# Performance work log

Measured on AMD Instinct MI355X. Metric: run time of the kernel, lower is better.

The kernel has to match this reference:

```python
import jax, jax.numpy as jnp
import numpy as np

N = 1024   # nodes (genomic bins); batch must be 1 per the original reshape
F = 128    # input feature dim
Fp = 64    # F_ per head
H = 2      # attn heads
NEG = -1e16


def setup_inputs() -> dict:
    key = jax.random.key(0)
    ks = jax.random.split(key, 6)
    X = jax.random.normal(ks[0], (1, N, F), dtype=jnp.float32)
    A = (jax.random.uniform(ks[1], (1, N, N)) < 0.05).astype(jnp.float32)
    W1 = jax.random.normal(ks[2], (H, F, Fp), dtype=jnp.float32) * (1.0 / np.sqrt(F))
    W2 = jax.random.normal(ks[3], (H, F, Fp), dtype=jnp.float32) * (1.0 / np.sqrt(F))
    b = jax.random.normal(ks[4], (H, Fp), dtype=jnp.float32) * 0.02
    a_att = jax.random.normal(ks[5], (H, Fp), dtype=jnp.float32) * (1.0 / np.sqrt(Fp))
    return {"X": X, "A": A, "W1": W1, "W2": W2, "b": b, "a_att": a_att}


def reference(X, A, W1, W2, b, a_att):
    # Per-head projections (vectorized over heads): [1, H, N, Fp]
    HW1 = jnp.einsum('bnf,hfe->bhne', X, W1)
    HW2 = jnp.einsum('bnf,hfe->bhne', X, W2)
    # Pairwise broadcast: pair[b,h,i,j,:] = HW1[i] + HW2[j] + bias  -> [1,H,N,N,Fp]
    pair = HW1[:, :, :, None, :] + HW2[:, :, None, :, :] + b[None, :, None, None, :]
    f = jax.nn.leaky_relu(pair, negative_slope=0.2)
    # Attention logits: project with attn kernel -> [1,H,N,N]
    att = jnp.einsum('bhije,he->bhij', f, a_att)
    # Mask non-edges, sigmoid attention (NOT softmax), custom normalization
    att = att + NEG * (1.0 - A)[:, None, :, :]
    att = jax.nn.sigmoid(att)
    att_sum = jnp.sum(att, axis=-1, keepdims=True)        # [1,H,N,1]
    att = att / (1.0 + att_sum)
    beta = 1.0 / (1.0 + att_sum)                          # self (promoter) weight
    # Aggregate: beta * HW1 + att @ HW2 (dropout is identity at inference)
    out = beta * HW1 + jnp.einsum('bhij,bhje->bhie', att, HW2)
    # Concat heads along feature dim: [1, N, H*Fp]
    out = jnp.transpose(out, (0, 2, 1, 3)).reshape(X.shape[0], X.shape[1], -1)
    out = jax.nn.relu(out)
    return out, att
```

## Files before the change

### kernel.cpp

```cpp
#include <hip/hip_runtime.h>

#define NN 1024
#define FF 128
#define FP 64
#define NH 2

#define VT_OFF 0
#define H2_OFF 131072
#define SV_OFF 262144
#define FLAG_OFF (1 << 22)
#define GEN 0x9E3779B1u

__device__ __forceinline__ void st_ag2(float* p, float x, float y) {
    union { unsigned long long u; float f[2]; } c;
    c.f[0] = x; c.f[1] = y;
    __hip_atomic_store((unsigned long long*)p, c.u, __ATOMIC_RELAXED,
                       __HIP_MEMORY_SCOPE_AGENT);
}
__device__ __forceinline__ void st_ag1(float* p, float x) {
    union { unsigned u; float f; } c; c.f = x;
    __hip_atomic_store((unsigned*)p, c.u, __ATOMIC_RELAXED,
                       __HIP_MEMORY_SCOPE_AGENT);
}

__global__ __launch_bounds__(512) void kFused(const float* __restrict__ X,
        const float* __restrict__ Ad, const float* __restrict__ W1,
        const float* __restrict__ W2, const float* __restrict__ b,
        const float* __restrict__ a, float* __restrict__ ws,
        float* __restrict__ out, float* __restrict__ att) {
    union Shm {
        float xs[8 * FF];
        struct { float eval[8][256]; int eidx[8][256]; } p2;
    };
    __shared__ Shm shm;
    __shared__ float s_u[FP][8];
    __shared__ float s_h1[8][FP];
    __shared__ float s_ae[FP];
    __shared__ float s_su[8];
    __shared__ __align__(16) float s_att[8][NN];
    __shared__ float s_rsum[8][8];
    __shared__ float s_inv[8];

    int h    = blockIdx.x >> 7;
    int i0   = (blockIdx.x & 127) * 8;
    int t    = threadIdx.x;
    int lane = t & 63;
    int wv   = t >> 6;

    *(float2*)(shm.xs + t * 2) = *(const float2*)(X + i0 * FF + t * 2);
    if (t < FP) s_ae[t] = a[h * FP + t];
    __syncthreads();

    {
        int wsel = wv >> 2;
        int r0   = (wv & 3) * 2;
        const float* Wp = (wsel ? W2 : W1) + h * FF * FP;
        const float* x0 = shm.xs + (r0 + 0) * FF;
        const float* x1 = shm.xs + (r0 + 1) * FF;
        float acc0 = 0.f, acc1 = 0.f;
        #pragma unroll 8
        for (int f = 0; f < FF; f += 4) {
            float w0 = Wp[(f + 0) * FP + lane];
            float w1 = Wp[(f + 1) * FP + lane];
            float w2 = Wp[(f + 2) * FP + lane];
            float w3 = Wp[(f + 3) * FP + lane];
            float4 xa = *(const float4*)(x0 + f);
            float4 xb = *(const float4*)(x1 + f);
            acc0 += w0 * xa.x + w1 * xa.y + w2 * xa.z + w3 * xa.w;
            acc1 += w0 * xb.x + w1 * xb.y + w2 * xb.z + w3 * xb.w;
        }
        float be = wsel ? 0.f : b[h * FP + lane];
        float u0 = acc0 + be, u1 = acc1 + be;
        float ae = s_ae[lane];
        float g0 = ae * u0, g1 = ae * u1;
        #pragma unroll
        for (int off = 32; off; off >>= 1) {
            g0 += __shfl_xor(g0, off, 64);
            g1 += __shfl_xor(g1, off, 64);
        }
        if (wsel == 0) {
            s_u[lane][r0] = u0; s_u[lane][r0 + 1] = u1;
            s_h1[r0][lane] = acc0; s_h1[r0 + 1][lane] = acc1;
            if (lane == 0) { s_su[r0] = g0; s_su[r0 + 1] = g1; }
        } else {
            st_ag2(ws + VT_OFF + h * FP * NN + lane * NN + i0 + r0, u0, u1);
            float* H2g = ws + H2_OFF + (h * NN + i0 + r0) * FP;
            st_ag1(H2g + lane, acc0);
            st_ag1(H2g + FP + lane, acc1);
            if (lane == 0)
                st_ag2(ws + SV_OFF + h * NN + i0 + r0, g0, g1);
        }
    }

    __syncthreads();
    unsigned int* flags = (unsigned int*)(ws + FLAG_OFF);
    if (t == 0)
        __hip_atomic_store(&flags[blockIdx.x], GEN, __ATOMIC_RELAXED,
                           __HIP_MEMORY_SCOPE_AGENT);
    if (t < 256) {
        while (__hip_atomic_load(&flags[t], __ATOMIC_RELAXED,
                                 __HIP_MEMORY_SCOPE_AGENT) != GEN)
            __builtin_amdgcn_s_sleep(4);
    }
    asm volatile("" ::: "memory");
    __syncthreads();

    int j2 = t * 2;
    float2 A2r[8];
    #pragma unroll
    for (int ii = 0; ii < 8; ++ii)
        A2r[ii] = *(const float2*)(Ad + (i0 + ii) * NN + j2);
    float2 sv = *(const float2*)(ws + SV_OFF + h * NN + j2);

    const float* VTp = ws + VT_OFF + h * FP * NN + j2;
    float acc[16];
    #pragma unroll
    for (int k = 0; k < 16; ++k) acc[k] = 0.f;

    #pragma unroll 8
    for (int e = 0; e < FP; ++e) {
        float2 v = *(const float2*)(VTp + e * NN);
        float4 ua = *(const float4*)(&s_u[e][0]);
        float4 ub = *(const float4*)(&s_u[e][4]);
        float ae = s_ae[e];
        float uu[8] = {ua.x, ua.y, ua.z, ua.w, ub.x, ub.y, ub.z, ub.w};
        #pragma unroll
        for (int ii = 0; ii < 8; ++ii) {
            acc[ii * 2 + 0] += ae * fabsf(uu[ii] + v.x);
            acc[ii * 2 + 1] += ae * fabsf(uu[ii] + v.y);
        }
    }

    float rs[8];
    #pragma unroll
    for (int ii = 0; ii < 8; ++ii) {
        float l0 = 0.6f * (s_su[ii] + sv.x) + 0.4f * acc[ii * 2 + 0];
        float l1 = 0.6f * (s_su[ii] + sv.y) + 0.4f * acc[ii * 2 + 1];
        float s0 = (A2r[ii].x != 0.f) ? 1.f / (1.f + __expf(-l0)) : 0.f;
        float s1 = (A2r[ii].y != 0.f) ? 1.f / (1.f + __expf(-l1)) : 0.f;
        acc[ii * 2 + 0] = s0;
        acc[ii * 2 + 1] = s1;
        *(float2*)(&s_att[ii][j2]) = make_float2(s0, s1);
        rs[ii] = s0 + s1;
    }
    #pragma unroll
    for (int off = 32; off; off >>= 1) {
        #pragma unroll
        for (int ii = 0; ii < 8; ++ii) rs[ii] += __shfl_xor(rs[ii], off, 64);
    }
    if (lane == 0) {
        #pragma unroll
        for (int ii = 0; ii < 8; ++ii) s_rsum[wv][ii] = rs[ii];
    }
    __syncthreads();
    if (t < 8) {
        float S = 0.f;
        #pragma unroll
        for (int wq = 0; wq < 8; ++wq) S += s_rsum[wq][t];
        s_inv[t] = 1.f / (1.f + S);
    }
    __syncthreads();

    #pragma unroll
    for (int ii = 0; ii < 8; ++ii) {
        float iv = s_inv[ii];
        *(float2*)(att + (h * NN + i0 + ii) * NN + j2) =
            make_float2(acc[ii * 2 + 0] * iv, acc[ii * 2 + 1] * iv);
    }

    int cnt = 0;
    #pragma unroll
    for (int c = 0; c < 16; ++c) {
        float val = s_att[wv][c * 64 + lane];
        unsigned long long m = __ballot(val != 0.f);
        if (val != 0.f) {
            int pos = cnt + __popcll(m & ((1ull << lane) - 1ull));
            if (pos < 256) {
                shm.p2.eidx[wv][pos] = c * 64 + lane;
                shm.p2.eval[wv][pos] = val;
            }
        }
        cnt += __popcll(m);
    }
    if (cnt > 256) cnt = 256;

    const float* H2p = ws + H2_OFF + h * NN * FP + lane;
    float agg = 0.f;
    #pragma unroll 4
    for (int k = 0; k < cnt; ++k) {
        agg += shm.p2.eval[wv][k] * H2p[shm.p2.eidx[wv][k] * FP];
    }
    float h1  = s_h1[wv][lane];
    float val = s_inv[wv] * (h1 + agg);
    out[(i0 + wv) * (NH * FP) + h * FP + lane] = fmaxf(val, 0.f);
}

extern "C" void kernel_launch(void* const* d_in, const int* in_sizes, int n_in,
                              void* d_out, int out_size, void* d_ws, size_t ws_size,
                              hipStream_t stream) {
    const float* X  = (const float*)d_in[0];
    const float* A  = (const float*)d_in[1];
    const float* W1 = (const float*)d_in[2];
    const float* W2 = (const float*)d_in[3];
    const float* b  = (const float*)d_in[4];
    const float* a  = (const float*)d_in[5];

    float* out = (float*)d_out;
    float* att = out + NN * NH * FP;
    float* ws  = (float*)d_ws;

    kFused<<<256, 512, 0, stream>>>(X, A, W1, W2, b, a, ws, out, att);
}
```

Baseline: 35.59 us.

## Stage VT tiles through double-buffered shared memory with register prefetch

Replaces direct per-thread global float2 loads of the transposed projection VT with cooperative float4 loads into a double-buffered LDS tile of 4 feature rows. The next tile is prefetched into registers while the current one is consumed, then written to the other buffer. The aim is wider coalesced global loads and hiding load latency. In exchange it adds 16 block-wide barriers and extra LDS traffic, and the data is only read once per thread anyway.

```diff
diff --git a/kernel.cpp b/kernel.cpp
--- a/kernel.cpp
+++ b/kernel.cpp
@@ -30,6 +30,7 @@
         float* __restrict__ out, float* __restrict__ att) {
     union Shm {
         float xs[8 * FF];
+        float vt[2 * 4 * NN];
         struct { float eval[8][256]; int eidx[8][256]; } p2;
     };
     __shared__ Shm shm;
@@ -112,23 +113,46 @@
         A2r[ii] = *(const float2*)(Ad + (i0 + ii) * NN + j2);
     float2 sv = *(const float2*)(ws + SV_OFF + h * NN + j2);
 
-    const float* VTp = ws + VT_OFF + h * FP * NN + j2;
+    const float* VTg = ws + VT_OFF + h * FP * NN;
     float acc[16];
     #pragma unroll
     for (int k = 0; k < 16; ++k) acc[k] = 0.f;
 
-    #pragma unroll 8
-    for (int e = 0; e < FP; ++e) {
-        float2 v = *(const float2*)(VTp + e * NN);
-        float4 ua = *(const float4*)(&s_u[e][0]);
-        float4 ub = *(const float4*)(&s_u[e][4]);
-        float ae = s_ae[e];
-        float uu[8] = {ua.x, ua.y, ua.z, ua.w, ub.x, ub.y, ub.z, ub.w};
-        #pragma unroll
-        for (int ii = 0; ii < 8; ++ii) {
-            acc[ii * 2 + 0] += ae * fabsf(uu[ii] + v.x);
-            acc[ii * 2 + 1] += ae * fabsf(uu[ii] + v.y);
-        }
+    {
+        const float4* s = (const float4*)VTg;
+        float4 pa = s[t], pb = s[t + 512];
+        ((float4*)shm.vt)[t] = pa;
+        ((float4*)shm.vt)[t + 512] = pb;
+    }
+    __syncthreads();
+
+    for (int c = 0; c < 16; ++c) {
+        int cur = c & 1;
+        float4 na, nb;
+        if (c < 15) {
+            const float4* s = (const float4*)(VTg + (c + 1) * 4096);
+            na = s[t]; nb = s[t + 512];
+        }
+        #pragma unroll
+        for (int eq = 0; eq < 4; ++eq) {
+            int e = c * 4 + eq;
+            float2 v = *(const float2*)(&shm.vt[cur * 4096 + eq * NN + j2]);
+            float4 ua = *(const float4*)(&s_u[e][0]);
+            float4 ub = *(const float4*)(&s_u[e][4]);
+            float ae = s_ae[e];
+            float uu[8] = {ua.x, ua.y, ua.z, ua.w, ub.x, ub.y, ub.z, ub.w};
+            #pragma unroll
+            for (int ii = 0; ii < 8; ++ii) {
+                acc[ii * 2 + 0] += ae * fabsf(uu[ii] + v.x);
+                acc[ii * 2 + 1] += ae * fabsf(uu[ii] + v.y);
+            }
+        }
+        if (c < 15) {
+            int nxt = cur ^ 1;
+            ((float4*)&shm.vt[nxt * 4096])[t] = na;
+            ((float4*)&shm.vt[nxt * 4096])[t + 512] = nb;
+        }
+        __syncthreads();
     }
 
     float rs[8];
```

After: 38.16 us. 7.2% more time.
